# Kernel tuning notes

Measured on AMD Instinct MI355X. Metric: run time of the kernel, lower is better.

The kernel has to match this reference:

```python
import jax, jax.numpy as jnp
import numpy as np

F_DIM = 128; K_RBF = 64; NBLOCKS = 3; NUM_SCC = 1; IBEGIN = 4
N_RES_INT = 2; N_RES_AT = 2; N_RES_OUT = 1
NUM_OUTPUTS = 2001; NOUTS = NUM_OUTPUTS + 4  # +4 charge-equilibration channels when num_scc>0
N_ATOMS = 10000; DEG = 32; N_EDGES = N_ATOMS * DEG; NMOL = 64
CUTOFF = 10.0
LOG2 = 0.6931471805599453


def ssp(x):
    # shifted softplus
    return jax.nn.softplus(x) - LOG2


def _residual(x, W1, b1, W2, b2):
    y = ssp(x) @ W1 + b1
    return x + ssp(y) @ W2 + b2


def _forward(R, M, QaAlpha, QaBeta,
             em_W0, em_b0, em_W1, em_b1, em_W2, em_b2,
             iWrbf, iWi, ibi, iWj, ibj, irW1, irb1, irW2, irb2, iWout, ibout, iu,
             arW1, arb1, arW2, arb2, orW1, orb1, orW2, orb2, oW,
             Z, idx_i, idx_j, mol_idx):
    N = R.shape[0]
    dt = R.dtype
    # --- interatomic distances via neighbor gather ---
    Dvec = R[idx_i] - R[idx_j]                                # [E,3]
    Dij = jnp.sqrt(jax.nn.relu(jnp.sum(Dvec * Dvec, -1)))     # [E]
    # --- PhysNet-style exp-Gaussian RBF expansion with smooth cutoff ---
    mu = jnp.linspace(np.exp(-CUTOFF), 1.0, K_RBF).astype(dt)
    gamma = jnp.asarray((K_RBF / (2.0 * (1.0 - np.exp(-CUTOFF)))) ** 2, dt)
    t = Dij / CUTOFF
    cut = jnp.where(Dij < CUTOFF, 1.0 - 6.0 * t**5 + 15.0 * t**4 - 10.0 * t**3, 0.0)
    rbf = cut[:, None] * jnp.exp(-gamma * (jnp.exp(-Dij)[:, None] - mu) ** 2)  # [E,K]

    seg_mol = lambda v: jax.ops.segment_sum(v, mol_idx, num_segments=NMOL)
    Zf = Z.astype(dt)[:, None]
    QaA, QaB = QaAlpha, QaBeta
    QAlpha_mol = seg_mol(QaA)
    QBeta_mol = seg_mol(QaB)
    outputs = None
    nhloss = jnp.asarray(0.0, dt)
    for j in range(NUM_SCC + 1):
        # elemental-modes embedding: f = [Z, M, QaAlpha, QaBeta] -> F
        f = jnp.concatenate([Zf, M[:, None], QaA[:, None], QaB[:, None]], 1)  # [N,4]
        h = ssp(f @ em_W0 + em_b0)
        h = ssp(h @ em_W1 + em_b1)
        x = h @ em_W2 + em_b2                                 # [N,F]
        outputs = jnp.zeros((N, NOUTS), dt)
        nhloss = jnp.asarray(0.0, dt)
        lastout2 = None
        for i in range(NBLOCKS):
            # --- interaction (message passing: gather -> multiply -> segment_sum) ---
            xa = ssp(x)
            g = rbf @ iWrbf[i]                                # [E,F]
            xi = ssp(xa @ iWi[i] + ibi[i])                    # [N,F]
            xj = ssp(xa @ iWj[i] + ibj[i])                    # [N,F]
            m = xi + jax.ops.segment_sum(g * xj[idx_j], idx_i, num_segments=N)
            for r in range(N_RES_INT):
                m = _residual(m, irW1[i, r], irb1[i, r], irW2[i, r], irb2[i, r])
            m = ssp(m)
            x = iu[i] * x + m @ iWout[i] + ibout[i]           # gated update
            for r in range(N_RES_AT):
                x = _residual(x, arW1[i, r], arb1[i, r], arW2[i, r], arb2[i, r])
            # --- output block ---
            xo = x
            for r in range(N_RES_OUT):
                xo = _residual(xo, orW1[i, r], orb1[i, r], orW2[i, r], orb2[i, r])
            out = ssp(xo) @ oW[i]                             # [N,NOUTS]
            outputs = outputs + out
            if j == NUM_SCC:
                out2 = out[IBEGIN:] ** 2                      # row slice, as in source
                if i > 0:
                    nhloss = nhloss + jnp.mean(out2 / (out2 + lastout2 + 1e-7))
                lastout2 = out2
        # --- NSE charge equilibration (per-molecule segment sums) ---
        QaA_n, faA = outputs[:, 0], outputs[:, 1]
        QaB_n, faB = outputs[:, 2], outputs[:, 3]
        QaA = QaA_n + faA * ((QAlpha_mol - seg_mol(QaA_n)) / seg_mol(faA))[mol_idx]
        QaB = QaB_n + faB * ((QBeta_mol - seg_mol(QaB_n)) / seg_mol(faB))[mol_idx]
    outputs = outputs[:, IBEGIN:]
    outputs = jnp.concatenate([outputs[:, :1], jax.nn.relu(outputs[:, 1:])], 1)
    return outputs, Dij, nhloss


def setup_inputs() -> dict:
    key = jax.random.key(0)
    ks = iter(jax.random.split(key, 64))
    nrm = lambda shp, scale: jax.random.normal(next(ks), shp, jnp.float32) * scale
    F, K, B = F_DIM, K_RBF, NBLOCKS
    s = F ** -0.5
    inp = {}
    inp["R"] = jax.random.uniform(next(ks), (N_ATOMS, 3), jnp.float32, 0.0, 12.0)
    inp["M"] = jax.random.uniform(next(ks), (N_ATOMS,), jnp.float32, 1.0, 32.0)
    inp["QaAlpha"] = nrm((N_ATOMS,), 0.1)
    inp["QaBeta"] = nrm((N_ATOMS,), 0.1)
    # elemental-modes MLP 4 -> F -> F -> F
    inp["em_W0"] = nrm((4, F), 0.5); inp["em_b0"] = nrm((F,), 0.01)
    inp["em_W1"] = nrm((F, F), s);   inp["em_b1"] = nrm((F,), 0.01)
    inp["em_W2"] = nrm((F, F), s);   inp["em_b2"] = nrm((F,), 0.01)
    # interaction blocks (stacked over NBLOCKS)
    inp["iWrbf"] = nrm((B, K, F), K ** -0.5)
    inp["iWi"] = nrm((B, F, F), s); inp["ibi"] = nrm((B, F), 0.01)
    inp["iWj"] = nrm((B, F, F), s); inp["ibj"] = nrm((B, F), 0.01)
    inp["irW1"] = nrm((B, N_RES_INT, F, F), s); inp["irb1"] = nrm((B, N_RES_INT, F), 0.01)
    inp["irW2"] = nrm((B, N_RES_INT, F, F), s); inp["irb2"] = nrm((B, N_RES_INT, F), 0.01)
    inp["iWout"] = nrm((B, F, F), s); inp["ibout"] = nrm((B, F), 0.01)
    inp["iu"] = jnp.ones((B, F), jnp.float32)
    inp["arW1"] = nrm((B, N_RES_AT, F, F), s); inp["arb1"] = nrm((B, N_RES_AT, F), 0.01)
    inp["arW2"] = nrm((B, N_RES_AT, F, F), s); inp["arb2"] = nrm((B, N_RES_AT, F), 0.01)
    inp["orW1"] = nrm((B, N_RES_OUT, F, F), s); inp["orb1"] = nrm((B, N_RES_OUT, F), 0.01)
    inp["orW2"] = nrm((B, N_RES_OUT, F, F), s); inp["orb2"] = nrm((B, N_RES_OUT, F), 0.01)
    inp["oW"] = nrm((B, F, NOUTS), s)
    # integer graph structure
    inp["Z"] = jax.random.randint(next(ks), (N_ATOMS,), 1, 36, jnp.int32)
    idx_i = jnp.repeat(jnp.arange(N_ATOMS, dtype=jnp.int32), DEG)
    rnd = jax.random.randint(next(ks), (N_EDGES,), 1, N_ATOMS, jnp.int32)
    inp["idx_i"] = idx_i
    inp["idx_j"] = (idx_i + rnd) % N_ATOMS  # never self -> Dij > 0
    inp["mol_idx"] = ((jnp.arange(N_ATOMS) * NMOL) // N_ATOMS).astype(jnp.int32)
    return inp


def reference(R, M, QaAlpha, QaBeta,
              em_W0, em_b0, em_W1, em_b1, em_W2, em_b2,
              iWrbf, iWi, ibi, iWj, ibj, irW1, irb1, irW2, irb2, iWout, ibout, iu,
              arW1, arb1, arW2, arb2, orW1, orb1, orW2, orb2, oW,
              Z, idx_i, idx_j, mol_idx):
    return _forward(R, M, QaAlpha, QaBeta,
                    em_W0, em_b0, em_W1, em_b1, em_W2, em_b2,
                    iWrbf, iWi, ibi, iWj, ibj, irW1, irb1, irW2, irb2, iWout, ibout, iu,
                    arW1, arb1, arW2, arb2, orW1, orb1, orW2, orb2, oW,
                    Z, idx_i, idx_j, mol_idx)
```

## Files before the change

### kernel.cpp

```cpp
#include <hip/hip_runtime.h>
#include <math.h>

#define NA 10000
#define FD 128
#define KR 64
#define DEGC 32
#define NE (NA*DEGC)
#define NOUTS_C 2005
#define NOUT_FINAL 2001

typedef __attribute__((ext_vector_type(8))) short bh8;
typedef __attribute__((ext_vector_type(4))) float fx4;

__device__ __forceinline__ float sspf(float x){
    float ex = __expf(-fabsf(x));
    return fmaxf(x, 0.0f) + __logf(1.0f + ex) - 0.6931471805599453f;
}
__device__ __forceinline__ unsigned short f2bf(float x){
    unsigned int u = __float_as_uint(x);
    unsigned int r = (u + 0x7fffu + ((u >> 16) & 1u)) >> 16;
    return (unsigned short)r;
}
__device__ __forceinline__ fx4 mfma16(bh8 a, bh8 b, fx4 c){
    return __builtin_amdgcn_mfma_f32_16x16x32_bf16(a, b, c, 0, 0, 0);
}
__device__ __forceinline__ void gll16(const void* g, void* l){
    __builtin_amdgcn_global_load_lds(
        (const __attribute__((address_space(1))) unsigned int*)g,
        (__attribute__((address_space(3))) unsigned int*)l, 16, 0, 0);
}

__global__ void k_dij(const float* __restrict__ R, const int* __restrict__ idx_i,
                      const int* __restrict__ idx_j, float* __restrict__ dij_out){
    int e = blockIdx.x*256 + threadIdx.x;
    if (e >= NE) return;
    int i = idx_i[e], j = idx_j[e];
    float dx = R[i*3+0] - R[j*3+0];
    float dy = R[i*3+1] - R[j*3+1];
    float dz = R[i*3+2] - R[j*3+2];
    dij_out[e] = sqrtf(fmaxf(dx*dx + dy*dy + dz*dz, 0.0f));
}

__global__ void k_rbf_bf(const float* __restrict__ dij_in, short* __restrict__ rbf_bf,
                         float gamma, float mu0, float dmu){
    int gid = blockIdx.x*256 + threadIdx.x;
    int e = gid >> 5, kp = (gid & 31)*2;
    float d = dij_in[e];
    float t = d * 0.1f;
    float cut = 0.0f;
    if (d < 10.0f){
        float t2 = t*t, t3 = t2*t, t4 = t2*t2, t5 = t4*t;
        cut = 1.0f - 6.0f*t5 + 15.0f*t4 - 10.0f*t3;
    }
    float ed = expf(-d);
    float u0 = ed - (mu0 + (float)kp*dmu);
    float u1 = ed - (mu0 + (float)(kp+1)*dmu);
    float v0 = cut * expf(-gamma*u0*u0);
    float v1 = cut * expf(-gamma*u1*u1);
    unsigned int pk = (unsigned int)f2bf(v0) | ((unsigned int)f2bf(v1) << 16);
    int idx = e*64 + (((kp>>3) ^ (e&7))*8) + (kp&7);
    *(unsigned int*)&rbf_bf[idx] = pk;
}

__global__ void k_init(const float* __restrict__ QaAin, const float* __restrict__ QaBin,
                       const int* __restrict__ mol, float* __restrict__ QaA,
                       float* __restrict__ QaB, float* __restrict__ QAmol,
                       float* __restrict__ QBmol){
    int a = blockIdx.x*256 + threadIdx.x;
    if (a >= NA) return;
    float qa = QaAin[a], qb = QaBin[a];
    QaA[a] = qa; QaB[a] = qb;
    int m = mol[a];
    atomicAdd(&QAmol[m], qa);
    atomicAdd(&QBmol[m], qb);
}

__global__ void k_cvtW(const float* __restrict__ em_W1, const float* __restrict__ em_W2,
                       const float* __restrict__ iWi, const float* __restrict__ iWj,
                       const float* __restrict__ iWout, const float* __restrict__ irW1,
                       const float* __restrict__ irW2, const float* __restrict__ arW1,
                       const float* __restrict__ arW2, const float* __restrict__ orW1,
                       const float* __restrict__ orW2, short* __restrict__ img){
    int gid = blockIdx.x*256 + threadIdx.x;
    if (gid >= 41*2048) return;
    int m = gid >> 11;
    int f = gid & 2047;
    int l15 = f & 15, t = f >> 4;
    int g = t & 3, u = t >> 2;
    int kk = u & 3, cg = u >> 2;
    const float* src; int mm;
    if      (m < 1){ src = em_W1; mm = m; }
    else if (m < 2){ src = em_W2; mm = m-1; }
    else if (m < 5){ src = iWi;   mm = m-2; }
    else if (m < 8){ src = iWj;   mm = m-5; }
    else if (m < 11){ src = iWout; mm = m-8; }
    else if (m < 17){ src = irW1;  mm = m-11; }
    else if (m < 23){ src = irW2;  mm = m-17; }
    else if (m < 29){ src = arW1;  mm = m-23; }
    else if (m < 35){ src = arW2;  mm = m-29; }
    else if (m < 38){ src = orW1;  mm = m-35; }
    else            { src = orW2;  mm = m-38; }
    src += (size_t)mm * 16384;
    int n = cg*16 + l15;
    int k0 = (kk*4 + g)*8;
    bh8 pk;
    #pragma unroll
    for (int j = 0; j < 8; ++j) pk[j] = (short)f2bf(src[(k0+j)*128 + n]);
    *(bh8*)&img[m*16384 + f*8] = pk;
}

__global__ void k_cvtB(const float* __restrict__ em_b1, const float* __restrict__ em_b2,
                       const float* __restrict__ ibi, const float* __restrict__ ibj,
                       const float* __restrict__ ibout, const float* __restrict__ irb1,
                       const float* __restrict__ irb2, const float* __restrict__ arb1,
                       const float* __restrict__ arb2, const float* __restrict__ orb1,
                       const float* __restrict__ orb2, const float* __restrict__ iu,
                       float* __restrict__ bimg){
    int gid = blockIdx.x*256 + threadIdx.x;
    if (gid >= 44*128) return;
    int m = gid >> 7, c = gid & 127;
    float v;
    if      (m < 1)  v = em_b1[c];
    else if (m < 2)  v = em_b2[c];
    else if (m < 5)  v = ibi[(m-2)*128+c];
    else if (m < 8)  v = ibj[(m-5)*128+c];
    else if (m < 11) v = ibout[(m-8)*128+c];
    else if (m < 17) v = irb1[(m-11)*128+c];
    else if (m < 23) v = irb2[(m-17)*128+c];
    else if (m < 29) v = arb1[(m-23)*128+c];
    else if (m < 35) v = arb2[(m-29)*128+c];
    else if (m < 38) v = orb1[(m-35)*128+c];
    else if (m < 41) v = orb2[(m-38)*128+c];
    else             v = iu[(m-41)*128+c];
    bimg[gid] = v;
}

__global__ void k_cvt_wrbf(const float* __restrict__ iWrbf, short* __restrict__ img){
    int gid = blockIdx.x*256 + threadIdx.x;
    if (gid >= 3*1024) return;
    int i = gid >> 10;
    int loc = gid & 1023;
    int n = loc >> 3, s = loc & 7;
    const float* src = iWrbf + (size_t)i*8192;
    int kbase = (s ^ (n&7)) * 8;
    bh8 pk;
    #pragma unroll
    for (int j = 0; j < 8; ++j) pk[j] = (short)f2bf(src[(kbase+j)*128 + n]);
    *(bh8*)&img[i*8192 + n*64 + s*8] = pk;
}

__global__ void k_cvt_oW(const float* __restrict__ oW, short* __restrict__ img){
    int gid = blockIdx.x*256 + threadIdx.x;
    if (gid >= 12*2048*4) return;
    int kk = gid >> 13;
    int loc = gid & 8191;
    int n = loc >> 2, s = loc & 3;
    int seg = kk >> 2;
    int kbase = (s ^ (n&3)) * 8;
    bh8 pk;
    #pragma unroll
    for (int j = 0; j < 8; ++j){
        int kseg = (kk&3)*32 + kbase + j;
        float v = (n < NOUTS_C) ? oW[((size_t)seg*128 + kseg)*NOUTS_C + n] : 0.0f;
        pk[j] = (short)f2bf(v);
    }
    *(bh8*)&img[((size_t)kk*2048 + n)*32 + s*8] = pk;
}

__device__ __forceinline__ void gemm16s(const short* As, const short* __restrict__ W,
                                        int g, int l15, int wv, fx4 acc[2]){
    const bh8* Wf = (const bh8*)W;
    const int cgA = wv*2, cgB = wv*2 + 1;
    bh8 b[8];
    #pragma unroll
    for (int kk = 0; kk < 4; ++kk){
        b[kk]   = Wf[((cgA*4+kk)*4+g)*16 + l15];
        b[4+kk] = Wf[((cgB*4+kk)*4+g)*16 + l15];
    }
    #pragma unroll
    for (int kk = 0; kk < 4; ++kk){
        int q = kk*4 + g;
        bh8 a = *(const bh8*)&As[l15*128 + ((q ^ (l15&7))*8)];
        acc[0] = mfma16(a, b[kk],   acc[0]);
        acc[1] = mfma16(a, b[4+kk], acc[1]);
    }
}
#define ZACC2 { acc[0]=(fx4){0,0,0,0}; acc[1]=(fx4){0,0,0,0}; }

__device__ __forceinline__ void epiS_ts(short* dst, fx4 acc[2], const float* b,
                                        int g, int c0, int c1){
    float b0 = b[c0], b1 = b[c1];
    #pragma unroll
    for (int r = 0; r < 4; ++r){
        int row = g*4 + r;
        dst[row*128 + (((c0>>3) ^ (row&7))*8) + (c0&7)] = (short)f2bf(sspf(acc[0][r] + b0));
        dst[row*128 + (((c1>>3) ^ (row&7))*8) + (c1&7)] = (short)f2bf(sspf(acc[1][r] + b1));
    }
}
__device__ __forceinline__ void epiS_xadd(float xr[2][4], fx4 acc[2], const float* b,
                                          int c0, int c1){
    float b0 = b[c0], b1 = b[c1];
    #pragma unroll
    for (int r = 0; r < 4; ++r){
        xr[0][r] += acc[0][r] + b0;
        xr[1][r] += acc[1][r] + b1;
    }
}
__device__ __forceinline__ void writeS_xr(short* dst, float xr[2][4], int g, int c0, int c1){
    #pragma unroll
    for (int r = 0; r < 4; ++r){
        int row = g*4 + r;
        dst[row*128 + (((c0>>3) ^ (row&7))*8) + (c0&7)] = (short)f2bf(sspf(xr[0][r]));
        dst[row*128 + (((c1>>3) ^ (row&7))*8) + (c1&7)] = (short)f2bf(sspf(xr[1][r]));
    }
}
__device__ __forceinline__ void storeS_xr(float* dst, float xr[2][4], int r0, int g, int c0, int c1){
    #pragma unroll
    for (int r = 0; r < 4; ++r){
        int row = r0 + g*4 + r;
        dst[(size_t)row*FD + c0] = xr[0][r];
        dst[(size_t)row*FD + c1] = xr[1][r];
    }
}
__device__ __forceinline__ void storeS_ssp(float* dst, fx4 acc[2], const float* b,
                                           int r0, int g, int c0, int c1){
    float b0 = b[c0], b1 = b[c1];
    #pragma unroll
    for (int r = 0; r < 4; ++r){
        int row = r0 + g*4 + r;
        dst[(size_t)row*FD + c0] = sspf(acc[0][r] + b0);
        dst[(size_t)row*FD + c1] = sspf(acc[1][r] + b1);
    }
}
__device__ __forceinline__ void stage_A16(short* As, const float* src, int r0, int tid){
    int row = tid >> 4, cb = tid & 15;
    const float* p = src + (size_t)(r0+row)*FD + cb*8;
    float4 u = *(const float4*)p, v = *(const float4*)(p+4);
    float vv[8] = {u.x,u.y,u.z,u.w,v.x,v.y,v.z,v.w};
    bh8 pk;
    #pragma unroll
    for (int t = 0; t < 8; ++t) pk[t] = (short)f2bf(sspf(vv[t]));
    *(bh8*)&As[row*128 + ((cb ^ (row&7))*8)] = pk;
}

__global__ __launch_bounds__(256) void k_pre(
    const short* __restrict__ wimg, const float* __restrict__ bimg,
    const int* __restrict__ Z, const float* __restrict__ M,
    const float* __restrict__ QaA, const float* __restrict__ QaB,
    const float* __restrict__ em_W0, const float* __restrict__ em_b0,
    float* __restrict__ x, float* __restrict__ xi, float* __restrict__ xj)
{
    __shared__ __align__(16) short As[2048];
    __shared__ __align__(16) short Ts[2048];
    __shared__ float fs[16][4];
    const int tid = threadIdx.x, wv = tid>>6, ln = tid&63, g = ln>>4, l15 = ln&15;
    const int r0 = blockIdx.x*16;
    const int c0 = wv*32 + l15, c1 = c0 + 16;
    if (tid < 64){
        int rr = tid>>2, k = tid&3;
        int a = r0 + rr;
        fs[rr][k] = (k==0) ? (float)Z[a] : (k==1) ? M[a] : (k==2) ? QaA[a] : QaB[a];
    }
    __syncthreads();
    {
        int row = tid>>4, cb = tid&15;
        bh8 pk;
        #pragma unroll
        for (int t = 0; t < 8; ++t){
            int c = cb*8 + t;
            float v = sspf(em_b0[c] + fs[row][0]*em_W0[c] + fs[row][1]*em_W0[128+c]
                           + fs[row][2]*em_W0[256+c] + fs[row][3]*em_W0[384+c]);
            pk[t] = (short)f2bf(v);
        }
        *(bh8*)&As[row*128 + ((cb ^ (row&7))*8)] = pk;
    }
    __syncthreads();
    fx4 acc[2];
    float xr[2][4];
    ZACC2; gemm16s(As, wimg + 0*16384, g, l15, wv, acc);
    epiS_ts(Ts, acc, bimg + 0*128, g, c0, c1);
    __syncthreads();
    ZACC2; gemm16s(Ts, wimg + 1*16384, g, l15, wv, acc);
    {
        const float* b = bimg + 1*128;
        float b0 = b[c0], b1 = b[c1];
        #pragma unroll
        for (int r = 0; r < 4; ++r){
            xr[0][r] = acc[0][r] + b0;
            xr[1][r] = acc[1][r] + b1;
        }
    }
    storeS_xr(x, xr, r0, g, c0, c1);
    writeS_xr(As, xr, g, c0, c1);
    __syncthreads();
    ZACC2; gemm16s(As, wimg + 2*16384, g, l15, wv, acc);
    storeS_ssp(xi, acc, bimg + 2*128, r0, g, c0, c1);
    ZACC2; gemm16s(As, wimg + 5*16384, g, l15, wv, acc);
    storeS_ssp(xj, acc, bimg + 5*128, r0, g, c0, c1);
}

__global__ __launch_bounds__(256) void k_post(
    const short* __restrict__ wimg, const float* __restrict__ bimg,
    const float* __restrict__ mb, float* __restrict__ x,
    float* __restrict__ xo, float* __restrict__ xi, float* __restrict__ xj,
    int i, int dodual)
{
    __shared__ __align__(16) short As[2048];
    __shared__ __align__(16) short Ts[2048];
    const int tid = threadIdx.x, wv = tid>>6, ln = tid&63, g = ln>>4, l15 = ln&15;
    const int r0 = blockIdx.x*16;
    const int c0 = wv*32 + l15, c1 = c0 + 16;
    float xr[2][4];
    #pragma unroll
    for (int r = 0; r < 4; ++r){
        size_t row = (size_t)(r0 + g*4 + r);
        xr[0][r] = mb[row*FD + c0];
        xr[1][r] = mb[row*FD + c1];
    }
    stage_A16(As, mb, r0, tid);
    __syncthreads();
    fx4 acc[2];
    ZACC2; gemm16s(As, wimg + (size_t)(11+2*i)*16384, g, l15, wv, acc);
    epiS_ts(Ts, acc, bimg + (11+2*i)*128, g, c0, c1);
    __syncthreads();
    ZACC2; gemm16s(Ts, wimg + (size_t)(17+2*i)*16384, g, l15, wv, acc);
    epiS_xadd(xr, acc, bimg + (17+2*i)*128, c0, c1);
    writeS_xr(As, xr, g, c0, c1);
    __syncthreads();
    ZACC2; gemm16s(As, wimg + (size_t)(12+2*i)*16384, g, l15, wv, acc);
    epiS_ts(Ts, acc, bimg + (12+2*i)*128, g, c0, c1);
    __syncthreads();
    ZACC2; gemm16s(Ts, wimg + (size_t)(18+2*i)*16384, g, l15, wv, acc);
    epiS_xadd(xr, acc, bimg + (18+2*i)*128, c0, c1);
    writeS_xr(As, xr, g, c0, c1);
    __syncthreads();
    ZACC2; gemm16s(As, wimg + (size_t)(8+i)*16384, g, l15, wv, acc);
    {
        const float* bb = bimg + (8+i)*128;
        const float* uu = bimg + (41+i)*128;
        float b0 = bb[c0], b1 = bb[c1], u0 = uu[c0], u1 = uu[c1];
        #pragma unroll
        for (int r = 0; r < 4; ++r){
            size_t row = (size_t)(r0 + g*4 + r);
            xr[0][r] = u0*x[row*FD + c0] + acc[0][r] + b0;
            xr[1][r] = u1*x[row*FD + c1] + acc[1][r] + b1;
        }
    }
    writeS_xr(Ts, xr, g, c0, c1);
    __syncthreads();
    ZACC2; gemm16s(Ts, wimg + (size_t)(23+2*i)*16384, g, l15, wv, acc);
    epiS_ts(As, acc, bimg + (23+2*i)*128, g, c0, c1);
    __syncthreads();
    ZACC2; gemm16s(As, wimg + (size_t)(29+2*i)*16384, g, l15, wv, acc);
    epiS_xadd(xr, acc, bimg + (29+2*i)*128, c0, c1);
    writeS_xr(Ts, xr, g, c0, c1);
    __syncthreads();
    ZACC2; gemm16s(Ts, wimg + (size_t)(24+2*i)*16384, g, l15, wv, acc);
    epiS_ts(As, acc, bimg + (24+2*i)*128, g, c0, c1);
    __syncthreads();
    ZACC2; gemm16s(As, wimg + (size_t)(30+2*i)*16384, g, l15, wv, acc);
    epiS_xadd(xr, acc, bimg + (30+2*i)*128, c0, c1);
    storeS_xr(x, xr, r0, g, c0, c1);
    writeS_xr(Ts, xr, g, c0, c1);
    __syncthreads();
    if (dodual){
        ZACC2; gemm16s(Ts, wimg + (size_t)(3+i)*16384, g, l15, wv, acc);
        storeS_ssp(xi, acc, bimg + (3+i)*128, r0, g, c0, c1);
        ZACC2; gemm16s(Ts, wimg + (size_t)(6+i)*16384, g, l15, wv, acc);
        storeS_ssp(xj, acc, bimg + (6+i)*128, r0, g, c0, c1);
    }
    ZACC2; gemm16s(Ts, wimg + (size_t)(35+i)*16384, g, l15, wv, acc);
    epiS_ts(As, acc, bimg + (35+i)*128, g, c0, c1);
    __syncthreads();
    ZACC2; gemm16s(As, wimg + (size_t)(38+i)*16384, g, l15, wv, acc);
    {
        const float* bb = bimg + (38+i)*128;
        float b0 = bb[c0], b1 = bb[c1];
        #pragma unroll
        for (int r = 0; r < 4; ++r){
            int row = r0 + g*4 + r;
            xo[(size_t)row*FD + c0] = xr[0][r] + acc[0][r] + b0;
            xo[(size_t)row*FD + c1] = xr[1][r] + acc[1][r] + b1;
        }
    }
}

__global__ __launch_bounds__(256) void k_agg_mfma(
    const short* __restrict__ rbf_bf, const short* __restrict__ wri,
    const int* __restrict__ idxj, const float* __restrict__ xi,
    const float* __restrict__ xj, float* __restrict__ mout)
{
    __shared__ short Rb[256*64];
    __shared__ short Wr[128*64];
    __shared__ int Jd[256];
    const int tid = threadIdx.x;
    const int wv = tid >> 6, ln = tid & 63;
    const int e0 = blockIdx.x * 256;
    {
        const char* g = (const char*)(rbf_bf + (size_t)e0*64);
        char* l = (char*)Rb;
        #pragma unroll
        for (int i = 0; i < 8; ++i){
            int off = wv*8192 + i*1024;
            gll16(g + off + ln*16, l + off);
        }
        const char* g2 = (const char*)wri;
        char* l2 = (char*)Wr;
        #pragma unroll
        for (int i = 0; i < 4; ++i){
            int off = wv*4096 + i*1024;
            gll16(g2 + off + ln*16, l2 + off);
        }
        Jd[tid] = idxj[e0 + tid];
    }
    __syncthreads();
    const int g = ln >> 4, l15 = ln & 15;
    bh8 a[4][2];
    #pragma unroll
    for (int mt = 0; mt < 4; ++mt){
        int el = wv*64 + mt*16 + l15;
        #pragma unroll
        for (int kk = 0; kk < 2; ++kk)
            a[mt][kk] = *(const bh8*)&Rb[el*64 + (((kk*4+g) ^ (el&7))*8)];
    }
    float pa[2][8];
    #pragma unroll
    for (int q = 0; q < 8; ++q){ pa[0][q]=0.f; pa[1][q]=0.f; }
    #pragma unroll
    for (int h = 0; h < 2; ++h){
        fx4 acc[4][4];
        #pragma unroll
        for (int mt = 0; mt < 4; ++mt)
            #pragma unroll
            for (int nt = 0; nt < 4; ++nt) acc[mt][nt] = (fx4){0,0,0,0};
        #pragma unroll
        for (int kk = 0; kk < 2; ++kk){
            #pragma unroll
            for (int nt = 0; nt < 4; ++nt){
                int n = h*64 + nt*16 + l15;
                bh8 b = *(const bh8*)&Wr[n*64 + (((kk*4+g) ^ (n&7))*8)];
                #pragma unroll
                for (int mt = 0; mt < 4; ++mt)
                    acc[mt][nt] = mfma16(a[mt][kk], b, acc[mt][nt]);
            }
        }
        #pragma unroll
        for (int mt = 0; mt < 4; ++mt){
            int at = mt >> 1;
            int jv[4];
            #pragma unroll
            for (int r = 0; r < 4; ++r) jv[r] = Jd[wv*64 + mt*16 + g*4 + r];
            #pragma unroll
            for (int nt = 0; nt < 4; ++nt){
                int col = h*64 + nt*16 + l15;
                float s = 0.f;
                #pragma unroll
                for (int r = 0; r < 4; ++r)
                    s += acc[mt][nt][r] * xj[(size_t)jv[r]*FD + col];
                pa[at][h*4+nt] += s;
            }
        }
    }
    #pragma unroll
    for (int at = 0; at < 2; ++at)
        #pragma unroll
        for (int q = 0; q < 8; ++q){
            float v = pa[at][q];
            v += __shfl_xor(v, 16);
            v += __shfl_xor(v, 32);
            pa[at][q] = v;
        }
    if (g == 0){
        #pragma unroll
        for (int at = 0; at < 2; ++at){
            int ga = blockIdx.x*8 + wv*2 + at;
            #pragma unroll
            for (int q = 0; q < 8; ++q){
                int col = (q>>2)*64 + (q&3)*16 + l15;
                mout[(size_t)ga*FD + col] = xi[(size_t)ga*FD + col] + pa[at][q];
            }
        }
    }
}

__global__ void k_out4all(const float* __restrict__ xo0, const float* __restrict__ xo1,
                          const float* __restrict__ xo2, const float* __restrict__ oW,
                          float* __restrict__ out4){
    int gid = blockIdx.x*256 + threadIdx.x;
    int a = gid >> 6;
    int lane = threadIdx.x & 63;
    if (a >= NA) return;
    float p0=0.f, p1=0.f, p2=0.f, p3=0.f;
    #pragma unroll
    for (int seg = 0; seg < 3; ++seg){
        const float* xo = (seg==0) ? xo0 : (seg==1) ? xo1 : xo2;
        const float* oWs = oW + (size_t)seg*FD*NOUTS_C;
        float y0 = sspf(xo[(size_t)a*FD + lane]);
        float y1 = sspf(xo[(size_t)a*FD + lane + 64]);
        const float* w0 = oWs + (size_t)lane*NOUTS_C;
        const float* w1 = oWs + (size_t)(lane+64)*NOUTS_C;
        p0 += y0*w0[0] + y1*w1[0];
        p1 += y0*w0[1] + y1*w1[1];
        p2 += y0*w0[2] + y1*w1[2];
        p3 += y0*w0[3] + y1*w1[3];
    }
    #pragma unroll
    for (int off = 32; off > 0; off >>= 1){
        p0 += __shfl_down(p0, off);
        p1 += __shfl_down(p1, off);
        p2 += __shfl_down(p2, off);
        p3 += __shfl_down(p3, off);
    }
    if (lane == 0){
        out4[a*4+0] = p0; out4[a*4+1] = p1;
        out4[a*4+2] = p2; out4[a*4+3] = p3;
    }
}

__global__ void k_molsum(const float* __restrict__ out4, const int* __restrict__ mol,
                         float* __restrict__ sums){
    int a = blockIdx.x*256 + threadIdx.x;
    if (a >= NA) return;
    int m = mol[a];
    atomicAdd(&sums[m],     out4[a*4+0]);
    atomicAdd(&sums[64+m],  out4[a*4+1]);
    atomicAdd(&sums[128+m], out4[a*4+2]);
    atomicAdd(&sums[192+m], out4[a*4+3]);
}

__global__ void k_qaupd(const float* __restrict__ out4, const int* __restrict__ mol,
                        const float* __restrict__ sums, const float* __restrict__ QAmol,
                        const float* __restrict__ QBmol, float* __restrict__ QaA,
                        float* __restrict__ QaB){
    int a = blockIdx.x*256 + threadIdx.x;
    if (a >= NA) return;
    int m = mol[a];
    float qa_n = out4[a*4+0], fa = out4[a*4+1];
    float qb_n = out4[a*4+2], fb = out4[a*4+3];
    QaA[a] = qa_n + fa * ((QAmol[m] - sums[m])     / sums[64+m]);
    QaB[a] = qb_n + fb * ((QBmol[m] - sums[128+m]) / sums[192+m]);
}

__global__ void k_prepA(const float* __restrict__ xo0, const float* __restrict__ xo1,
                        const float* __restrict__ xo2, short* __restrict__ Aimg){
    int gid = blockIdx.x*256 + threadIdx.x;
    if (gid >= 10048*48) return;
    int row = gid / 48, s = gid - row*48;
    bh8 pk;
    if (row < NA){
        int seg = s >> 4, kl = (s & 15)*8;
        const float* src = ((seg==0) ? xo0 : (seg==1) ? xo1 : xo2) + (size_t)row*FD + kl;
        float4 u = *(const float4*)src;
        float4 v = *(const float4*)(src + 4);
        pk[0]=(short)f2bf(sspf(u.x)); pk[1]=(short)f2bf(sspf(u.y));
        pk[2]=(short)f2bf(sspf(u.z)); pk[3]=(short)f2bf(sspf(u.w));
        pk[4]=(short)f2bf(sspf(v.x)); pk[5]=(short)f2bf(sspf(v.y));
        pk[6]=(short)f2bf(sspf(v.z)); pk[7]=(short)f2bf(sspf(v.w));
    } else {
        #pragma unroll
        for (int j = 0; j < 8; ++j) pk[j] = 0;
    }
    *(bh8*)&Aimg[(size_t)row*384 + ((s ^ (row&7))*8)] = pk;
}

__global__ __launch_bounds__(256) void k_final2(
    const short* __restrict__ Aimg, const short* __restrict__ oWimg,
    float* __restrict__ outp, float* __restrict__ nh_acc)
{
    __shared__ __align__(16) short As[64*384];
    __shared__ __align__(16) short Bs[12*128*32];
    const int tid = threadIdx.x, wv = tid>>6, ln = tid&63, g = ln>>4, l15 = ln&15;
    const int cg = blockIdx.x;
    const int a0 = blockIdx.y * 64;
    {
        const char* gA = (const char*)(Aimg + (size_t)a0*384);
        char* lA = (char*)As;
        #pragma unroll
        for (int i = 0; i < 12; ++i){
            int off = wv*12288 + i*1024;
            gll16(gA + off + ln*16, lA + off);
        }
        const char* gB = (const char*)oWimg;
        char* lB = (char*)Bs;
        #pragma unroll
        for (int kk = 0; kk < 12; ++kk)
            #pragma unroll
            for (int i = 0; i < 2; ++i){
                gll16(gB + kk*131072 + cg*8192 + wv*2048 + i*1024 + ln*16,
                      lB + kk*8192 + wv*2048 + i*1024);
            }
    }
    __syncthreads();
    const int arow = wv*16 + l15;
    fx4 osum[8], p2[8];
    #pragma unroll
    for (int nt = 0; nt < 8; ++nt){ osum[nt] = (fx4){0,0,0,0}; p2[nt] = (fx4){0,0,0,0}; }
    float nh = 0.f;
    for (int seg = 0; seg < 3; ++seg){
        fx4 acc[8];
        #pragma unroll
        for (int nt = 0; nt < 8; ++nt) acc[nt] = (fx4){0,0,0,0};
        #pragma unroll
        for (int kkl = 0; kkl < 4; ++kkl){
            int kk2 = seg*4 + kkl;
            int s = kk2*4 + g;
            bh8 a = *(const bh8*)&As[arow*384 + ((s ^ (arow&7))*8)];
            #pragma unroll
            for (int nt = 0; nt < 8; ++nt){
                int n = nt*16 + l15;
                bh8 b = *(const bh8*)&Bs[kk2*4096 + n*32 + ((g ^ (n&3))*8)];
                acc[nt] = mfma16(a, b, acc[nt]);
            }
        }
        #pragma unroll
        for (int nt = 0; nt < 8; ++nt)
        #pragma unroll
        for (int r = 0; r < 4; ++r){
            float o = acc[nt][r];
            osum[nt][r] += o;
            if (seg > 0){
                int A = a0 + wv*16 + g*4 + r;
                int col = cg*128 + nt*16 + l15;
                if (A >= 4 && A < NA && col < NOUTS_C){
                    float o2 = o*o;
                    float den = o2 + p2[nt][r] + 1e-7f;
                    float rr;
                    asm("v_rcp_f32 %0, %1" : "=v"(rr) : "v"(den));
                    nh += o2 * rr;
                }
            }
            p2[nt][r] = o*o;
        }
    }
    #pragma unroll
    for (int nt = 0; nt < 8; ++nt){
        int col = cg*128 + nt*16 + l15;
        #pragma unroll
        for (int r = 0; r < 4; ++r){
            int A = a0 + wv*16 + g*4 + r;
            if (A < NA && col >= 4 && col < NOUTS_C){
                float v = osum[nt][r];
                if (col > 4) v = fmaxf(v, 0.f);
                outp[(size_t)A*NOUT_FINAL + (col - 4)] = v;
            }
        }
    }
    #pragma unroll
    for (int off = 32; off > 0; off >>= 1) nh += __shfl_down(nh, off);
    if (ln == 0) atomicAdd(nh_acc, nh);
}

__global__ void k_finalize(const float* __restrict__ nh_acc, float* __restrict__ nh_out){
    *nh_out = *nh_acc * (1.0f / (float)((NA - 4) * NOUTS_C));
}

extern "C" void kernel_launch(void* const* d_in, const int* in_sizes, int n_in,
                              void* d_out, int out_size, void* d_ws, size_t ws_size,
                              hipStream_t stream)
{
    const float* R       = (const float*)d_in[0];
    const float* M       = (const float*)d_in[1];
    const float* QaAlpha = (const float*)d_in[2];
    const float* QaBeta  = (const float*)d_in[3];
    const float* em_W0   = (const float*)d_in[4];
    const float* em_b0   = (const float*)d_in[5];
    const float* em_W1   = (const float*)d_in[6];
    const float* em_b1   = (const float*)d_in[7];
    const float* em_W2   = (const float*)d_in[8];
    const float* em_b2   = (const float*)d_in[9];
    const float* iWrbf   = (const float*)d_in[10];
    const float* iWi     = (const float*)d_in[11];
    const float* ibi     = (const float*)d_in[12];
    const float* iWj     = (const float*)d_in[13];
    const float* ibj     = (const float*)d_in[14];
    const float* irW1    = (const float*)d_in[15];
    const float* irb1    = (const float*)d_in[16];
    const float* irW2    = (const float*)d_in[17];
    const float* irb2    = (const float*)d_in[18];
    const float* iWout   = (const float*)d_in[19];
    const float* ibout   = (const float*)d_in[20];
    const float* iu      = (const float*)d_in[21];
    const float* arW1    = (const float*)d_in[22];
    const float* arb1    = (const float*)d_in[23];
    const float* arW2    = (const float*)d_in[24];
    const float* arb2    = (const float*)d_in[25];
    const float* orW1    = (const float*)d_in[26];
    const float* orb1    = (const float*)d_in[27];
    const float* orW2    = (const float*)d_in[28];
    const float* orb2    = (const float*)d_in[29];
    const float* oW      = (const float*)d_in[30];
    const int*   Z       = (const int*)d_in[31];
    const int*   idx_i   = (const int*)d_in[32];
    const int*   idx_j   = (const int*)d_in[33];
    const int*   mol     = (const int*)d_in[34];

    float* out    = (float*)d_out;
    float* dij    = out + (size_t)NA*NOUT_FINAL;
    float* nh_out = dij + NE;

    float* fbase = (float*)d_ws;
    size_t fo = 0;
    float* x    = fbase + fo; fo += (size_t)NA*FD;
    float* xi   = fbase + fo; fo += (size_t)NA*FD;
    float* xj   = fbase + fo; fo += (size_t)NA*FD;
    float* mb   = fbase + fo; fo += (size_t)NA*FD;
    float* xo0  = fbase + fo; fo += (size_t)NA*FD;
    float* xo1  = fbase + fo; fo += (size_t)NA*FD;
    float* xo2  = fbase + fo; fo += (size_t)NA*FD;
    float* out4 = fbase + fo; fo += (size_t)NA*4;
    float* sums = fbase + fo; fo += 256;
    float* QAmol= fbase + fo; fo += 64;
    float* QBmol= fbase + fo; fo += 64;
    float* nhac = fbase + fo; fo += 1;
    float* QaA  = fbase + fo; fo += NA;
    float* QaB  = fbase + fo; fo += NA;
    float* bimg = fbase + fo; fo += 44*128;
    size_t sboff = ((fo*4 + 63) / 64) * 64;
    short* sbase = (short*)((char*)d_ws + sboff);
    size_t so = 0;
    short* rbf_bf = sbase + so; so += (size_t)NE*64;
    short* wimg   = sbase + so; so += (size_t)41*16384;
    short* wrbf   = sbase + so; so += (size_t)3*8192;
    short* oWimg  = sbase + so; so += (size_t)12*2048*32;
    short* Aimg   = sbase + so; so += (size_t)10048*384;

    hipMemsetAsync(sums, 0, (size_t)(256 + 64 + 64 + 1)*sizeof(float), stream);

    k_cvtW<<<(41*2048+255)/256, 256, 0, stream>>>(em_W1, em_W2, iWi, iWj, iWout,
                                                  irW1, irW2, arW1, arW2, orW1, orW2, wimg);
    k_cvtB<<<(44*128+255)/256, 256, 0, stream>>>(em_b1, em_b2, ibi, ibj, ibout,
                                                 irb1, irb2, arb1, arb2, orb1, orb2, iu, bimg);
    k_cvt_wrbf<<<(3*1024+255)/256, 256, 0, stream>>>(iWrbf, wrbf);
    k_cvt_oW<<<(12*2048*4)/256, 256, 0, stream>>>(oW, oWimg);

    k_dij<<<(NE+255)/256, 256, 0, stream>>>(R, idx_i, idx_j, dij);
    {
        double expn = exp(-10.0);
        float gamma = (float)pow(64.0/(2.0*(1.0-expn)), 2.0);
        float mu0 = (float)expn;
        float dmu = (float)((1.0-expn)/63.0);
        k_rbf_bf<<<(NE*32)/256, 256, 0, stream>>>(dij, rbf_bf, gamma, mu0, dmu);
    }
    k_init<<<(NA+255)/256, 256, 0, stream>>>(QaAlpha, QaBeta, mol, QaA, QaB, QAmol, QBmol);

    for (int j = 0; j <= 1; ++j){
        k_pre<<<625, 256, 0, stream>>>(wimg, bimg, Z, M, QaA, QaB, em_W0, em_b0, x, xi, xj);
        for (int i = 0; i < 3; ++i){
            k_agg_mfma<<<1250, 256, 0, stream>>>(rbf_bf, wrbf + (size_t)i*8192, idx_j, xi, xj, mb);
            float* xo = (i==0) ? xo0 : (i==1) ? xo1 : xo2;
            k_post<<<625, 256, 0, stream>>>(wimg, bimg, mb, x, xo, xi, xj, i, (i<2) ? 1 : 0);
        }
        if (j == 0){
            k_out4all<<<(NA*64)/256, 256, 0, stream>>>(xo0, xo1, xo2, oW, out4);
            k_molsum<<<(NA+255)/256, 256, 0, stream>>>(out4, mol, sums);
            k_qaupd<<<(NA+255)/256, 256, 0, stream>>>(out4, mol, sums, QAmol, QBmol, QaA, QaB);
        }
    }
    k_prepA<<<(10048*48)/256, 256, 0, stream>>>(xo0, xo1, xo2, Aimg);
    k_final2<<<dim3(16,157), 256, 0, stream>>>(Aimg, oWimg, out, nhac);
    k_finalize<<<1, 1, 0, stream>>>(nhac, nh_out);
}
```

Baseline: 982.9 us.

## Fuse RBF into aggregation, write bf16 Aimg from post, prefetch weights, fragment-layout oW

Several changes land together. RBF features are now computed inside the aggregation kernel, so the large bf16 RBF buffer is no longer written and read from global memory. The post kernel writes ssp-activated bf16 outputs straight into the final GEMM's A image, which removes the xo buffers and the prepA kernel. The dense layers prefetch the next weight fragments into registers while the current MFMA runs. The final GEMM reads oW in a precomputed fragment layout directly from global memory instead of staging it in LDS, with the grid order swapped. The cost is recomputing the exponentials on every block and every pass, plus higher register pressure, and k_out4all now reads bf16-rounded activations.

```diff
diff --git a/kernel.cpp b/kernel.cpp
--- a/kernel.cpp
+++ b/kernel.cpp
@@ -20,6 +20,9 @@
     unsigned int u = __float_as_uint(x);
     unsigned int r = (u + 0x7fffu + ((u >> 16) & 1u)) >> 16;
     return (unsigned short)r;
+}
+__device__ __forceinline__ float bf2f(unsigned short u){
+    return __uint_as_float(((unsigned int)u) << 16);
 }
 __device__ __forceinline__ fx4 mfma16(bh8 a, bh8 b, fx4 c){
     return __builtin_amdgcn_mfma_f32_16x16x32_bf16(a, b, c, 0, 0, 0);
@@ -39,27 +42,6 @@
     float dy = R[i*3+1] - R[j*3+1];
     float dz = R[i*3+2] - R[j*3+2];
     dij_out[e] = sqrtf(fmaxf(dx*dx + dy*dy + dz*dz, 0.0f));
-}
-
-__global__ void k_rbf_bf(const float* __restrict__ dij_in, short* __restrict__ rbf_bf,
-                         float gamma, float mu0, float dmu){
-    int gid = blockIdx.x*256 + threadIdx.x;
-    int e = gid >> 5, kp = (gid & 31)*2;
-    float d = dij_in[e];
-    float t = d * 0.1f;
-    float cut = 0.0f;
-    if (d < 10.0f){
-        float t2 = t*t, t3 = t2*t, t4 = t2*t2, t5 = t4*t;
-        cut = 1.0f - 6.0f*t5 + 15.0f*t4 - 10.0f*t3;
-    }
-    float ed = expf(-d);
-    float u0 = ed - (mu0 + (float)kp*dmu);
-    float u1 = ed - (mu0 + (float)(kp+1)*dmu);
-    float v0 = cut * expf(-gamma*u0*u0);
-    float v1 = cut * expf(-gamma*u1*u1);
-    unsigned int pk = (unsigned int)f2bf(v0) | ((unsigned int)f2bf(v1) << 16);
-    int idx = e*64 + (((kp>>3) ^ (e&7))*8) + (kp&7);
-    *(unsigned int*)&rbf_bf[idx] = pk;
 }
 
 __global__ void k_init(const float* __restrict__ QaAin, const float* __restrict__ QaBin,
@@ -151,32 +133,34 @@
 
 __global__ void k_cvt_oW(const float* __restrict__ oW, short* __restrict__ img){
     int gid = blockIdx.x*256 + threadIdx.x;
-    if (gid >= 12*2048*4) return;
-    int kk = gid >> 13;
-    int loc = gid & 8191;
-    int n = loc >> 2, s = loc & 3;
-    int seg = kk >> 2;
-    int kbase = (s ^ (n&3)) * 8;
+    if (gid >= 98304) return;
+    int l15 = gid & 15;
+    int g = (gid >> 4) & 3;
+    int nt = (gid >> 6) & 7;
+    int rest = gid >> 9;
+    int kk2 = rest % 12, cg = rest / 12;
+    int seg = kk2 >> 2;
+    int n = cg*128 + nt*16 + l15;
+    int kbase = (kk2 & 3)*32 + g*8;
     bh8 pk;
     #pragma unroll
     for (int j = 0; j < 8; ++j){
-        int kseg = (kk&3)*32 + kbase + j;
-        float v = (n < NOUTS_C) ? oW[((size_t)seg*128 + kseg)*NOUTS_C + n] : 0.0f;
+        float v = (n < NOUTS_C) ? oW[((size_t)seg*128 + kbase + j)*NOUTS_C + n] : 0.0f;
         pk[j] = (short)f2bf(v);
     }
-    *(bh8*)&img[((size_t)kk*2048 + n)*32 + s*8] = pk;
-}
-
-__device__ __forceinline__ void gemm16s(const short* As, const short* __restrict__ W,
-                                        int g, int l15, int wv, fx4 acc[2]){
+    *(bh8*)&img[(size_t)gid*8] = pk;
+}
+
+__device__ __forceinline__ void loadB8(const short* __restrict__ W, int g, int l15, int wv, bh8 b[8]){
     const bh8* Wf = (const bh8*)W;
     const int cgA = wv*2, cgB = wv*2 + 1;
-    bh8 b[8];
     #pragma unroll
     for (int kk = 0; kk < 4; ++kk){
         b[kk]   = Wf[((cgA*4+kk)*4+g)*16 + l15];
         b[4+kk] = Wf[((cgB*4+kk)*4+g)*16 + l15];
     }
+}
+__device__ __forceinline__ void gemmB(const short* As, const bh8 b[8], int g, int l15, fx4 acc[2]){
     #pragma unroll
     for (int kk = 0; kk < 4; ++kk){
         int q = kk*4 + g;
@@ -256,6 +240,7 @@
     const int tid = threadIdx.x, wv = tid>>6, ln = tid&63, g = ln>>4, l15 = ln&15;
     const int r0 = blockIdx.x*16;
     const int c0 = wv*32 + l15, c1 = c0 + 16;
+    bh8 bU[8], bV[8];
     if (tid < 64){
         int rr = tid>>2, k = tid&3;
         int a = r0 + rr;
@@ -274,13 +259,16 @@
         }
         *(bh8*)&As[row*128 + ((cb ^ (row&7))*8)] = pk;
     }
+    loadB8(wimg + 0*16384, g, l15, wv, bU);
     __syncthreads();
     fx4 acc[2];
     float xr[2][4];
-    ZACC2; gemm16s(As, wimg + 0*16384, g, l15, wv, acc);
+    ZACC2; gemmB(As, bU, g, l15, acc);
+    loadB8(wimg + 1*16384, g, l15, wv, bV);
     epiS_ts(Ts, acc, bimg + 0*128, g, c0, c1);
     __syncthreads();
-    ZACC2; gemm16s(Ts, wimg + 1*16384, g, l15, wv, acc);
+    ZACC2; gemmB(Ts, bV, g, l15, acc);
+    loadB8(wimg + 2*16384, g, l15, wv, bU);
     {
         const float* b = bimg + 1*128;
         float b0 = b[c0], b1 = b[c1];
@@ -293,16 +281,17 @@
     storeS_xr(x, xr, r0, g, c0, c1);
     writeS_xr(As, xr, g, c0, c1);
     __syncthreads();
-    ZACC2; gemm16s(As, wimg + 2*16384, g, l15, wv, acc);
+    ZACC2; gemmB(As, bU, g, l15, acc);
+    loadB8(wimg + 5*16384, g, l15, wv, bV);
     storeS_ssp(xi, acc, bimg + 2*128, r0, g, c0, c1);
-    ZACC2; gemm16s(As, wimg + 5*16384, g, l15, wv, acc);
+    ZACC2; gemmB(As, bV, g, l15, acc);
     storeS_ssp(xj, acc, bimg + 5*128, r0, g, c0, c1);
 }
 
 __global__ __launch_bounds__(256) void k_post(
     const short* __restrict__ wimg, const float* __restrict__ bimg,
     const float* __restrict__ mb, float* __restrict__ x,
-    float* __restrict__ xo, float* __restrict__ xi, float* __restrict__ xj,
+    short* __restrict__ Aimg, float* __restrict__ xi, float* __restrict__ xj,
     int i, int dodual)
 {
     __shared__ __align__(16) short As[2048];
@@ -310,6 +299,7 @@
     const int tid = threadIdx.x, wv = tid>>6, ln = tid&63, g = ln>>4, l15 = ln&15;
     const int r0 = blockIdx.x*16;
     const int c0 = wv*32 + l15, c1 = c0 + 16;
+    bh8 bU[8], bV[8];
     float xr[2][4];
     #pragma unroll
     for (int r = 0; r < 4; ++r){
@@ -318,23 +308,29 @@
         xr[1][r] = mb[row*FD + c1];
     }
     stage_A16(As, mb, r0, tid);
+    loadB8(wimg + (size_t)(11+2*i)*16384, g, l15, wv, bU);
     __syncthreads();
     fx4 acc[2];
-    ZACC2; gemm16s(As, wimg + (size_t)(11+2*i)*16384, g, l15, wv, acc);
+    ZACC2; gemmB(As, bU, g, l15, acc);
+    loadB8(wimg + (size_t)(17+2*i)*16384, g, l15, wv, bV);
     epiS_ts(Ts, acc, bimg + (11+2*i)*128, g, c0, c1);
     __syncthreads();
-    ZACC2; gemm16s(Ts, wimg + (size_t)(17+2*i)*16384, g, l15, wv, acc);
+    ZACC2; gemmB(Ts, bV, g, l15, acc);
+    loadB8(wimg + (size_t)(12+2*i)*16384, g, l15, wv, bU);
     epiS_xadd(xr, acc, bimg + (17+2*i)*128, c0, c1);
     writeS_xr(As, xr, g, c0, c1);
     __syncthreads();
-    ZACC2; gemm16s(As, wimg + (size_t)(12+2*i)*16384, g, l15, wv, acc);
+    ZACC2; gemmB(As, bU, g, l15, acc);
+    loadB8(wimg + (size_t)(18+2*i)*16384, g, l15, wv, bV);
     epiS_ts(Ts, acc, bimg + (12+2*i)*128, g, c0, c1);
     __syncthreads();
-    ZACC2; gemm16s(Ts, wimg + (size_t)(18+2*i)*16384, g, l15, wv, acc);
+    ZACC2; gemmB(Ts, bV, g, l15, acc);
+    loadB8(wimg + (size_t)(8+i)*16384, g, l15, wv, bU);
     epiS_xadd(xr, acc, bimg + (18+2*i)*128, c0, c1);
     writeS_xr(As, xr, g, c0, c1);
     __syncthreads();
-    ZACC2; gemm16s(As, wimg + (size_t)(8+i)*16384, g, l15, wv, acc);
+    ZACC2; gemmB(As, bU, g, l15, acc);
+    loadB8(wimg + (size_t)(23+2*i)*16384, g, l15, wv, bV);
     {
         const float* bb = bimg + (8+i)*128;
         const float* uu = bimg + (41+i)*128;
@@ -348,47 +344,62 @@
     }
     writeS_xr(Ts, xr, g, c0, c1);
     __syncthreads();
-    ZACC2; gemm16s(Ts, wimg + (size_t)(23+2*i)*16384, g, l15, wv, acc);
+    ZACC2; gemmB(Ts, bV, g, l15, acc);
+    loadB8(wimg + (size_t)(29+2*i)*16384, g, l15, wv, bU);
     epiS_ts(As, acc, bimg + (23+2*i)*128, g, c0, c1);
     __syncthreads();
-    ZACC2; gemm16s(As, wimg + (size_t)(29+2*i)*16384, g, l15, wv, acc);
+    ZACC2; gemmB(As, bU, g, l15, acc);
+    loadB8(wimg + (size_t)(24+2*i)*16384, g, l15, wv, bV);
     epiS_xadd(xr, acc, bimg + (29+2*i)*128, c0, c1);
     writeS_xr(Ts, xr, g, c0, c1);
     __syncthreads();
-    ZACC2; gemm16s(Ts, wimg + (size_t)(24+2*i)*16384, g, l15, wv, acc);
+    ZACC2; gemmB(Ts, bV, g, l15, acc);
+    loadB8(wimg + (size_t)(30+2*i)*16384, g, l15, wv, bU);
     epiS_ts(As, acc, bimg + (24+2*i)*128, g, c0, c1);
     __syncthreads();
-    ZACC2; gemm16s(As, wimg + (size_t)(30+2*i)*16384, g, l15, wv, acc);
+    ZACC2; gemmB(As, bU, g, l15, acc);
+    loadB8(wimg + (size_t)(dodual ? (3+i) : (35+i))*16384, g, l15, wv, bV);
     epiS_xadd(xr, acc, bimg + (30+2*i)*128, c0, c1);
     storeS_xr(x, xr, r0, g, c0, c1);
     writeS_xr(Ts, xr, g, c0, c1);
     __syncthreads();
     if (dodual){
-        ZACC2; gemm16s(Ts, wimg + (size_t)(3+i)*16384, g, l15, wv, acc);
+        ZACC2; gemmB(Ts, bV, g, l15, acc);
+        loadB8(wimg + (size_t)(6+i)*16384, g, l15, wv, bU);
         storeS_ssp(xi, acc, bimg + (3+i)*128, r0, g, c0, c1);
-        ZACC2; gemm16s(Ts, wimg + (size_t)(6+i)*16384, g, l15, wv, acc);
+        ZACC2; gemmB(Ts, bU, g, l15, acc);
+        loadB8(wimg + (size_t)(35+i)*16384, g, l15, wv, bV);
         storeS_ssp(xj, acc, bimg + (6+i)*128, r0, g, c0, c1);
-    }
-    ZACC2; gemm16s(Ts, wimg + (size_t)(35+i)*16384, g, l15, wv, acc);
-    epiS_ts(As, acc, bimg + (35+i)*128, g, c0, c1);
-    __syncthreads();
-    ZACC2; gemm16s(As, wimg + (size_t)(38+i)*16384, g, l15, wv, acc);
+        ZACC2; gemmB(Ts, bV, g, l15, acc);
+        loadB8(wimg + (size_t)(38+i)*16384, g, l15, wv, bU);
+        epiS_ts(As, acc, bimg + (35+i)*128, g, c0, c1);
+    } else {
+        ZACC2; gemmB(Ts, bV, g, l15, acc);
+        loadB8(wimg + (size_t)(38+i)*16384, g, l15, wv, bU);
+        epiS_ts(As, acc, bimg + (35+i)*128, g, c0, c1);
+    }
+    __syncthreads();
+    ZACC2; gemmB(As, bU, g, l15, acc);
     {
         const float* bb = bimg + (38+i)*128;
         float b0 = bb[c0], b1 = bb[c1];
         #pragma unroll
         for (int r = 0; r < 4; ++r){
             int row = r0 + g*4 + r;
-            xo[(size_t)row*FD + c0] = xr[0][r] + acc[0][r] + b0;
-            xo[(size_t)row*FD + c1] = xr[1][r] + acc[1][r] + b1;
+            float v0 = xr[0][r] + acc[0][r] + b0;
+            float v1 = xr[1][r] + acc[1][r] + b1;
+            int k0 = i*128 + c0, k1 = i*128 + c1;
+            Aimg[(size_t)row*384 + (((k0>>3) ^ (row&7))*8) + (k0&7)] = (short)f2bf(sspf(v0));
+            Aimg[(size_t)row*384 + (((k1>>3) ^ (row&7))*8) + (k1&7)] = (short)f2bf(sspf(v1));
         }
     }
 }
 
 __global__ __launch_bounds__(256) void k_agg_mfma(
-    const short* __restrict__ rbf_bf, const short* __restrict__ wri,
+    const float* __restrict__ dij, const short* __restrict__ wri,
     const int* __restrict__ idxj, const float* __restrict__ xi,
-    const float* __restrict__ xj, float* __restrict__ mout)
+    const float* __restrict__ xj, float* __restrict__ mout,
+    float gamma, float mu0, float dmu)
 {
     __shared__ short Rb[256*64];
     __shared__ short Wr[128*64];
@@ -397,13 +408,6 @@
     const int wv = tid >> 6, ln = tid & 63;
     const int e0 = blockIdx.x * 256;
     {
-        const char* g = (const char*)(rbf_bf + (size_t)e0*64);
-        char* l = (char*)Rb;
-        #pragma unroll
-        for (int i = 0; i < 8; ++i){
-            int off = wv*8192 + i*1024;
-            gll16(g + off + ln*16, l + off);
-        }
         const char* g2 = (const char*)wri;
         char* l2 = (char*)Wr;
         #pragma unroll
@@ -412,6 +416,27 @@
             gll16(g2 + off + ln*16, l2 + off);
         }
         Jd[tid] = idxj[e0 + tid];
+    }
+    {
+        float d = dij[e0 + tid];
+        float t = d * 0.1f;
+        float cut = 0.0f;
+        if (d < 10.0f){
+            float t2 = t*t, t3 = t2*t, t4 = t2*t2, t5 = t4*t;
+            cut = 1.0f - 6.0f*t5 + 15.0f*t4 - 10.0f*t3;
+        }
+        float ed = __expf(-d);
+        int row = tid;
+        #pragma unroll
+        for (int s = 0; s < 8; ++s){
+            bh8 pk;
+            #pragma unroll
+            for (int jj = 0; jj < 8; ++jj){
+                float u = ed - (mu0 + (float)(s*8+jj)*dmu);
+                pk[jj] = (short)f2bf(cut * __expf(-gamma*u*u));
+            }
+            *(bh8*)&Rb[row*64 + ((s ^ (row&7))*8)] = pk;
+        }
     }
     __syncthreads();
     const int g = ln >> 4, l15 = ln & 15;
@@ -483,8 +508,7 @@
     }
 }
 
-__global__ void k_out4all(const float* __restrict__ xo0, const float* __restrict__ xo1,
-                          const float* __restrict__ xo2, const float* __restrict__ oW,
+__global__ void k_out4all(const short* __restrict__ Aimg, const float* __restrict__ oW,
                           float* __restrict__ out4){
     int gid = blockIdx.x*256 + threadIdx.x;
     int a = gid >> 6;
@@ -493,10 +517,10 @@
     float p0=0.f, p1=0.f, p2=0.f, p3=0.f;
     #pragma unroll
     for (int seg = 0; seg < 3; ++seg){
-        const float* xo = (seg==0) ? xo0 : (seg==1) ? xo1 : xo2;
         const float* oWs = oW + (size_t)seg*FD*NOUTS_C;
-        float y0 = sspf(xo[(size_t)a*FD + lane]);
-        float y1 = sspf(xo[(size_t)a*FD + lane + 64]);
+        int k0 = seg*128 + lane, k1 = k0 + 64;
+        float y0 = bf2f((unsigned short)Aimg[(size_t)a*384 + (((k0>>3) ^ (a&7))*8) + (k0&7)]);
+        float y1 = bf2f((unsigned short)Aimg[(size_t)a*384 + (((k1>>3) ^ (a&7))*8) + (k1&7)]);
         const float* w0 = oWs + (size_t)lane*NOUTS_C;
         const float* w1 = oWs + (size_t)(lane+64)*NOUTS_C;
         p0 += y0*w0[0] + y1*w1[0];
@@ -541,37 +565,14 @@
     QaB[a] = qb_n + fb * ((QBmol[m] - sums[128+m]) / sums[192+m]);
 }
 
-__global__ void k_prepA(const float* __restrict__ xo0, const float* __restrict__ xo1,
-                        const float* __restrict__ xo2, short* __restrict__ Aimg){
-    int gid = blockIdx.x*256 + threadIdx.x;
-    if (gid >= 10048*48) return;
-    int row = gid / 48, s = gid - row*48;
-    bh8 pk;
-    if (row < NA){
-        int seg = s >> 4, kl = (s & 15)*8;
-        const float* src = ((seg==0) ? xo0 : (seg==1) ? xo1 : xo2) + (size_t)row*FD + kl;
-        float4 u = *(const float4*)src;
-        float4 v = *(const float4*)(src + 4);
-        pk[0]=(short)f2bf(sspf(u.x)); pk[1]=(short)f2bf(sspf(u.y));
-        pk[2]=(short)f2bf(sspf(u.z)); pk[3]=(short)f2bf(sspf(u.w));
-        pk[4]=(short)f2bf(sspf(v.x)); pk[5]=(short)f2bf(sspf(v.y));
-        pk[6]=(short)f2bf(sspf(v.z)); pk[7]=(short)f2bf(sspf(v.w));
-    } else {
-        #pragma unroll
-        for (int j = 0; j < 8; ++j) pk[j] = 0;
-    }
-    *(bh8*)&Aimg[(size_t)row*384 + ((s ^ (row&7))*8)] = pk;
-}
-
-__global__ __launch_bounds__(256) void k_final2(
-    const short* __restrict__ Aimg, const short* __restrict__ oWimg,
+__global__ __launch_bounds__(256) void k_final3(
+    const short* __restrict__ Aimg, const short* __restrict__ oWfrag,
     float* __restrict__ outp, float* __restrict__ nh_acc)
 {
     __shared__ __align__(16) short As[64*384];
-    __shared__ __align__(16) short Bs[12*128*32];
     const int tid = threadIdx.x, wv = tid>>6, ln = tid&63, g = ln>>4, l15 = ln&15;
-    const int cg = blockIdx.x;
-    const int a0 = blockIdx.y * 64;
+    const int a0 = blockIdx.x * 64;
+    const int cg = blockIdx.y;
     {
         const char* gA = (const char*)(Aimg + (size_t)a0*384);
         char* lA = (char*)As;
@@ -580,17 +581,9 @@
             int off = wv*12288 + i*1024;
             gll16(gA + off + ln*16, lA + off);
         }
-        const char* gB = (const char*)oWimg;
-        char* lB = (char*)Bs;
-        #pragma unroll
-        for (int kk = 0; kk < 12; ++kk)
-            #pragma unroll
-            for (int i = 0; i < 2; ++i){
-                gll16(gB + kk*131072 + cg*8192 + wv*2048 + i*1024 + ln*16,
-                      lB + kk*8192 + wv*2048 + i*1024);
-            }
-    }
-    __syncthreads();
+    }
+    __syncthreads();
+    const bh8* Bf = (const bh8*)oWfrag + (size_t)cg*12*8*64;
     const int arow = wv*16 + l15;
     fx4 osum[8], p2[8];
     #pragma unroll
@@ -603,14 +596,15 @@
         #pragma unroll
         for (int kkl = 0; kkl < 4; ++kkl){
             int kk2 = seg*4 + kkl;
+            bh8 b[8];
+            #pragma unroll
+            for (int nt = 0; nt < 8; ++nt)
+                b[nt] = Bf[((size_t)kk2*8 + nt)*64 + g*16 + l15];
             int s = kk2*4 + g;
             bh8 a = *(const bh8*)&As[arow*384 + ((s ^ (arow&7))*8)];
             #pragma unroll
-            for (int nt = 0; nt < 8; ++nt){
-                int n = nt*16 + l15;
-                bh8 b = *(const bh8*)&Bs[kk2*4096 + n*32 + ((g ^ (n&3))*8)];
-                acc[nt] = mfma16(a, b, acc[nt]);
-            }
+            for (int nt = 0; nt < 8; ++nt)
+                acc[nt] = mfma16(a, b[nt], acc[nt]);
         }
         #pragma unroll
         for (int nt = 0; nt < 8; ++nt)
@@ -704,9 +698,6 @@
     float* xi   = fbase + fo; fo += (size_t)NA*FD;
     float* xj   = fbase + fo; fo += (size_t)NA*FD;
     float* mb   = fbase + fo; fo += (size_t)NA*FD;
-    float* xo0  = fbase + fo; fo += (size_t)NA*FD;
-    float* xo1  = fbase + fo; fo += (size_t)NA*FD;
-    float* xo2  = fbase + fo; fo += (size_t)NA*FD;
     float* out4 = fbase + fo; fo += (size_t)NA*4;
     float* sums = fbase + fo; fo += 256;
     float* QAmol= fbase + fo; fo += 64;
@@ -718,45 +709,42 @@
     size_t sboff = ((fo*4 + 63) / 64) * 64;
     short* sbase = (short*)((char*)d_ws + sboff);
     size_t so = 0;
-    short* rbf_bf = sbase + so; so += (size_t)NE*64;
     short* wimg   = sbase + so; so += (size_t)41*16384;
     short* wrbf   = sbase + so; so += (size_t)3*8192;
-    short* oWimg  = sbase + so; so += (size_t)12*2048*32;
+    short* oWfrag = sbase + so; so += (size_t)98304*8;
     short* Aimg   = sbase + so; so += (size_t)10048*384;
 
     hipMemsetAsync(sums, 0, (size_t)(256 + 64 + 64 + 1)*sizeof(float), stream);
+    hipMemsetAsync(Aimg + (size_t)10000*384, 0, (size_t)48*384*sizeof(short), stream);
 
     k_cvtW<<<(41*2048+255)/256, 256, 0, stream>>>(em_W1, em_W2, iWi, iWj, iWout,
                                                   irW1, irW2, arW1, arW2, orW1, orW2, wimg);
     k_cvtB<<<(44*128+255)/256, 256, 0, stream>>>(em_b1, em_b2, ibi, ibj, ibout,
                                                  irb1, irb2, arb1, arb2, orb1, orb2, iu, bimg);
     k_cvt_wrbf<<<(3*1024+255)/256, 256, 0, stream>>>(iWrbf, wrbf);
-    k_cvt_oW<<<(12*2048*4)/256, 256, 0, stream>>>(oW, oWimg);
+    k_cvt_oW<<<(98304+255)/256, 256, 0, stream>>>(oW, oWfrag);
 
     k_dij<<<(NE+255)/256, 256, 0, stream>>>(R, idx_i, idx_j, dij);
-    {
-        double expn = exp(-10.0);
-        float gamma = (float)pow(64.0/(2.0*(1.0-expn)), 2.0);
-        float mu0 = (float)expn;
-        float dmu = (float)((1.0-expn)/63.0);
-        k_rbf_bf<<<(NE*32)/256, 256, 0, stream>>>(dij, rbf_bf, gamma, mu0, dmu);
-    }
     k_init<<<(NA+255)/256, 256, 0, stream>>>(QaAlpha, QaBeta, mol, QaA, QaB, QAmol, QBmol);
+
+    double expn = exp(-10.0);
+    float gamma = (float)pow(64.0/(2.0*(1.0-expn)), 2.0);
+    float mu0 = (float)expn;
+    float dmu = (float)((1.0-expn)/63.0);
 
     for (int j = 0; j <= 1; ++j){
         k_pre<<<625, 256, 0, stream>>>(wimg, bimg, Z, M, QaA, QaB, em_W0, em_b0, x, xi, xj);
         for (int i = 0; i < 3; ++i){
-            k_agg_mfma<<<1250, 256, 0, stream>>>(rbf_bf, wrbf + (size_t)i*8192, idx_j, xi, xj, mb);
-            float* xo = (i==0) ? xo0 : (i==1) ? xo1 : xo2;
-            k_post<<<625, 256, 0, stream>>>(wimg, bimg, mb, x, xo, xi, xj, i, (i<2) ? 1 : 0);
+            k_agg_mfma<<<1250, 256, 0, stream>>>(dij, wrbf + (size_t)i*8192, idx_j, xi, xj, mb,
+                                                 gamma, mu0, dmu);
+            k_post<<<625, 256, 0, stream>>>(wimg, bimg, mb, x, Aimg, xi, xj, i, (i<2) ? 1 : 0);
         }
         if (j == 0){
-            k_out4all<<<(NA*64)/256, 256, 0, stream>>>(xo0, xo1, xo2, oW, out4);
+            k_out4all<<<(NA*64)/256, 256, 0, stream>>>(Aimg, oW, out4);
             k_molsum<<<(NA+255)/256, 256, 0, stream>>>(out4, mol, sums);
             k_qaupd<<<(NA+255)/256, 256, 0, stream>>>(out4, mol, sums, QAmol, QBmol, QaA, QaB);
         }
     }
-    k_prepA<<<(10048*48)/256, 256, 0, stream>>>(xo0, xo1, xo2, Aimg);
-    k_final2<<<dim3(16,157), 256, 0, stream>>>(Aimg, oWimg, out, nhac);
+    k_final3<<<dim3(157,16), 256, 0, stream>>>(Aimg, oWfrag, out, nhac);
     k_finalize<<<1, 1, 0, stream>>>(nhac, nh_out);
 }
```

After: 963.6 us. -2.0%, faster.
